# Performance work log

Hardware: AMD Instinct MI355X
Metric: run time of the kernel (lower is better)

## Reference

```python
import jax, jax.numpy as jnp
import numpy as np

K = 3      # kernel_size
PAD = 1    # padding
HID = 64   # hidden
EPS = 1e-5

def _unfold(x, H, W):
    # x: (B, CT, H, W) -> (B, CT, K*K, H*W); matches torch nn.Unfold channel-major layout
    xp = jnp.pad(x, ((0, 0), (0, 0), (PAD, PAD), (PAD, PAD)))
    patches = jnp.stack([xp[:, :, i:i + H, j:j + W]
                         for i in range(K) for j in range(K)], axis=2)
    B, CT = x.shape[:2]
    return patches.reshape(B, CT, K * K, H * W)

def _fold(y, H, W):
    # y: (B, CT, K*K, H*W) -> scatter-add overlapping patches -> (B, CT, H, W); matches F.fold
    B, CT = y.shape[:2]
    y = y.reshape(B, CT, K * K, H, W)
    out = jnp.zeros((B, CT, H + 2 * PAD, W + 2 * PAD), y.dtype)
    idx = 0
    for i in range(K):
        for j in range(K):
            out = out.at[:, :, i:i + H, j:j + W].add(y[:, :, idx])
            idx += 1
    return out[:, :, PAD:PAD + H, PAD:PAD + W]

def setup_inputs() -> dict:
    key = jax.random.key(0)
    ks = jax.random.split(key, 4)
    B, C, T, H, W = 8, 64, 4, 56, 56
    return {
        "x": jax.random.normal(ks[0], (B, C, T, H, W), jnp.float32),
        "w_in": jax.random.normal(ks[1], (3 * HID, C), jnp.float32) * (C ** -0.5),
        "b_in": jnp.zeros((3 * HID,), jnp.float32),
        "w_out": jax.random.normal(ks[2], (C, HID), jnp.float32) * (HID ** -0.5),
        "b_out": jnp.zeros((C,), jnp.float32),
        "gamma": jnp.ones((C,), jnp.float32),
        "beta": jnp.zeros((C,), jnp.float32),
    }

def reference(x, w_in, b_in, w_out, b_out, gamma, beta):
    B, C, T, H, W = x.shape
    k2 = K * K
    # 1x1x1 conv_in -> theta, phi, g
    h = jnp.einsum('oc,bcthw->bothw', w_in, x) + b_in[None, :, None, None, None]
    theta, phi, g = jnp.split(h, 3, axis=1)

    def unf(z):  # (B, HID, T, H, W) -> (B, HID, T*k2, H*W)
        z = z.reshape(B, HID * T, H, W)
        return _unfold(z, H, W).reshape(B, HID, T * k2, H * W)

    tu, pu, gu = unf(theta), unf(phi), unf(g)
    # per-spatial-location attention over T*k2 axis; dot_product normalization
    attn = jnp.einsum('bcts,bcps->btps', tu, pu) / (T * k2)
    out = jnp.einsum('btgs,bcgs->bcts', attn, gu)      # (B, HID, T*k2, H*W)
    out = out.reshape(B, HID * T, k2, H * W)
    out = _fold(out, H, W).reshape(B, HID, T, H, W)
    # 1x1x1 conv_out
    out = jnp.einsum('oc,bcthw->bothw', w_out, out) + b_out[None, :, None, None, None]
    # BatchNorm3d (training-mode batch statistics, biased variance)
    mu = out.mean(axis=(0, 2, 3, 4), keepdims=True)
    var = out.var(axis=(0, 2, 3, 4), keepdims=True)
    out = (out - mu) * jax.lax.rsqrt(var + EPS)
    out = out * gamma[None, :, None, None, None] + beta[None, :, None, None, None]
    return x + out
```

## Files before the change

kernel.cpp:

```cpp
#include <hip/hip_runtime.h>


typedef unsigned short u16;
typedef unsigned int u32;
using f32x4 = __attribute__((ext_vector_type(4))) float;
using bf16x8 = __attribute__((ext_vector_type(8))) short;

#define BB 8
#define TT 4
#define HH 56
#define HWD 3136
#define GROW 64
#define GPLANE 3584
#define NTOT 100352.0f

__device__ __forceinline__ float bf_lo(u32 u) { return __uint_as_float(u << 16); }
__device__ __forceinline__ float bf_hi(u32 u) { return __uint_as_float(u & 0xffff0000u); }
__device__ __forceinline__ float bf16u(u16 u) { return __uint_as_float(((u32)u) << 16); }
__device__ __forceinline__ u16 f2bf(float f) {
  u32 u = __float_as_uint(f);
  u32 r = (u + 0x7fffu + ((u >> 16) & 1u)) >> 16;
  return (u16)r;
}
__device__ __forceinline__ u32 pack2(float a, float b) {
  return (u32)f2bf(a) | ((u32)f2bf(b) << 16);
}
__device__ __forceinline__ int imax(int a, int b) { return a > b ? a : b; }
__device__ __forceinline__ int imin(int a, int b) { return a < b ? a : b; }
__device__ __forceinline__ float cntf(int d, int p) {
  int lo = imax(-1, imax(-1 - d, p - (HH - 1)));
  int hi = imin(1, imin(1 - d, p));
  int n = hi - lo + 1;
  return n > 0 ? (float)n : 0.f;
}

#define K1_XOFF 24576
__global__ __launch_bounds__(256, 4) void k_conv_in(const float* __restrict__ x,
                                                    const float* __restrict__ w_in,
                                                    const float* __restrict__ b_in,
                                                    u16* __restrict__ th, u16* __restrict__ ph,
                                                    u16* __restrict__ g2, float* __restrict__ stats) {
  __shared__ __align__(16) char sm[24576 + 8192];
  if (blockIdx.x == 0 && threadIdx.x < 128) stats[threadIdx.x] = 0.f;
  int bi0 = blockIdx.x;
  int bi = (bi0 & 7) * 196 + (bi0 >> 3);
  int bt = bi / 49, chunk = bi % 49;
  int b = bt >> 2, t = bt & 3;
  int p0 = chunk * 64;
  int tid = threadIdx.x;

#pragma unroll
  for (int it = 0; it < 12; ++it) {
    int task = it * 256 + tid;
    int o = task >> 4, c4 = (task & 15) * 4;
    float4 wv = *reinterpret_cast<const float4*>(&w_in[o * 64 + c4]);
    uint2 pv;
    pv.x = pack2(wv.x, wv.y);
    pv.y = pack2(wv.z, wv.w);
    *reinterpret_cast<uint2*>(sm + o * 128 + ((c4 * 2) ^ ((o & 7) << 4))) = pv;
  }
  const float* xb = x + ((size_t)b * 256 + t) * HWD + p0;
#pragma unroll
  for (int it = 0; it < 2; ++it) {
    int task = it * 256 + tid;
    int cp = task >> 4, p4 = task & 15;
    int c0 = cp * 2;
    float4 fa = *reinterpret_cast<const float4*>(&xb[(size_t)c0 * 4 * HWD + p4 * 4]);
    float4 fb = *reinterpret_cast<const float4*>(&xb[(size_t)(c0 + 1) * 4 * HWD + p4 * 4]);
    float va[4] = {fa.x, fa.y, fa.z, fa.w}, vb[4] = {fb.x, fb.y, fb.z, fb.w};
#pragma unroll
    for (int j = 0; j < 4; ++j) {
      int p = p4 * 4 + j;
      int slot = (p & 7) ^ ((p >> 2) & 7);
      *reinterpret_cast<u32*>(sm + K1_XOFF + p * 128 + ((c0 * 2) ^ (slot << 4))) = pack2(va[j], vb[j]);
    }
  }
  __syncthreads();

  int w = tid >> 6, lane = tid & 63, lr = lane & 15, lk = lane >> 4;
  f32x4 acc[3][4];
#pragma unroll
  for (int i = 0; i < 3; ++i)
#pragma unroll
    for (int n = 0; n < 4; ++n) acc[i][n] = (f32x4){0.f, 0.f, 0.f, 0.f};

#pragma unroll
  for (int kt = 0; kt < 2; ++kt) {
    bf16x8 af[3], bfr[4];
#pragma unroll
    for (int i = 0; i < 3; ++i) {
      int arow = (w * 3 + i) * 16 + lr;
      af[i] = *reinterpret_cast<const bf16x8*>(sm + arow * 128 + ((kt * 64 + lk * 16) ^ ((arow & 7) << 4)));
    }
#pragma unroll
    for (int n = 0; n < 4; ++n) {
      int brow = n * 16 + lr;
      int slot = (brow & 7) ^ ((brow >> 2) & 7);
      bfr[n] = *reinterpret_cast<const bf16x8*>(sm + K1_XOFF + brow * 128 + ((kt * 64 + lk * 16) ^ (slot << 4)));
    }
#pragma unroll
    for (int i = 0; i < 3; ++i)
#pragma unroll
      for (int n = 0; n < 4; ++n)
        acc[i][n] = __builtin_amdgcn_mfma_f32_16x16x32_bf16(af[i], bfr[n], acc[i][n], 0, 0, 0);
  }

#pragma unroll
  for (int i = 0; i < 3; ++i) {
    int mt = w * 3 + i;
    int ob = mt * 16 + lk * 4;
    int gsel = ob >> 6, o = ob & 63;
    float4 bv = *reinterpret_cast<const float4*>(&b_in[ob]);
    if (gsel < 2) {
      u16* og = gsel == 0 ? th : ph;
#pragma unroll
      for (int n = 0; n < 4; ++n) {
        int p = p0 + n * 16 + lr;
        f32x4 a = acc[i][n];
        uint2 v;
        v.x = pack2(a.x + bv.x, a.y + bv.y);
        v.y = pack2(a.z + bv.z, a.w + bv.w);
        *reinterpret_cast<uint2*>(&og[((size_t)bt * HWD + p) * 64 + o]) = v;
      }
    } else {
      float bb[4] = {bv.x, bv.y, bv.z, bv.w};
      int y0p = p0 / 56;
      int rel0 = p0 - y0p * 56;
#pragma unroll
      for (int n = 0; n < 4; ++n) {
        f32x4 a = acc[i][n];
        float aa[4] = {a.x, a.y, a.z, a.w};
        int rel = rel0 + n * 16 + lr;
        int cnd = rel >= 56;
        int off = (y0p + cnd) * GROW + (rel - (cnd ? 56 : 0)) + 2;
#pragma unroll
        for (int r = 0; r < 4; ++r)
          g2[(((size_t)b * 64 + o + r) * 4 + t) * GPLANE + off] = f2bf(aa[r] + bb[r]);
      }
    }
  }
}

#define PH_OFF 0
#define AS_OFF 0
#define G_OFF 32768
#define TH_OFF 65536
#define FOLD_OFF 65536
#define W_OFF 73728

__global__ __launch_bounds__(512, 4) void k_attn(const u16* __restrict__ th, const u16* __restrict__ ph,
                                                 const u16* __restrict__ g2,
                                                 const float* __restrict__ w_out,
                                                 const float* __restrict__ b_out,
                                                 u16* __restrict__ pre) {
  __shared__ __align__(16) char sm[81920];

  int bi0 = blockIdx.x;
  int bi = (bi0 & 7) * 196 + (bi0 >> 3);
  int b = bi / 196, tile = bi % 196;
  int ty = tile / 14, tx = tile % 14;
  int y0 = ty * 4, x0 = tx * 4;
  int tid = threadIdx.x;
  int w = tid >> 6, lane = tid & 63;
  int lr = lane & 15, lk = lane >> 4;

  for (int task = tid; task < 2048; task += 512) {
    int row = task >> 3, ch = task & 7;
    int rho = row >> 6, Z = row & 63, zy = Z >> 3, zx = Z & 7;
    int Y = y0 - 2 + zy, X = x0 - 2 + zx;
    uint4 v = make_uint4(0, 0, 0, 0);
    if ((unsigned)Y < HH && (unsigned)X < HH)
      v = *reinterpret_cast<const uint4*>(&ph[(((size_t)b * 4 + rho) * HWD + Y * HH + X) * 64 + ch * 8]);
    *reinterpret_cast<uint4*>(sm + PH_OFF + row * 128 + ((ch * 16) ^ ((row & 7) << 4))) = v;
  }
  {
    int row = tid >> 3, ch = tid & 7;
    int pos = row >> 2, tau = row & 3;
    int Y = y0 + (pos >> 2), X = x0 + (pos & 3);
    uint4 v = *reinterpret_cast<const uint4*>(&th[(((size_t)b * 4 + tau) * HWD + Y * HH + X) * 64 + ch * 8]);
    *reinterpret_cast<uint4*>(sm + TH_OFF + row * 128 + ((ch * 16) ^ ((row & 7) << 4))) = v;
  }
  for (int task = tid; task < 2048; task += 512) {
    int c = task >> 5, rho = (task >> 3) & 3, zy = task & 7;
    int Y = y0 - 2 + zy;
    uint2 lo = make_uint2(0, 0), hi = make_uint2(0, 0);
    if ((unsigned)Y < HH) {
      const u16* gb = g2 + (((size_t)b * 64 + c) * 4 + rho) * GPLANE + Y * GROW + x0;
      lo = *reinterpret_cast<const uint2*>(gb);
      hi = *reinterpret_cast<const uint2*>(gb + 4);
    }
    uint4 v = make_uint4(lo.x, lo.y, hi.x, hi.y);
    *reinterpret_cast<uint4*>(sm + G_OFF + c * 512 + ((16 * (rho * 8 + zy)) ^ ((c & 7) << 4))) = v;
  }
  {
    int o = tid >> 3, cg = tid & 7;
    float4 w0 = *reinterpret_cast<const float4*>(&w_out[o * 64 + cg * 8]);
    float4 w1 = *reinterpret_cast<const float4*>(&w_out[o * 64 + cg * 8 + 4]);
    uint4 wv = make_uint4(pack2(w0.x, w0.y), pack2(w0.z, w0.w), pack2(w1.x, w1.y), pack2(w1.z, w1.w));
    *reinterpret_cast<uint4*>(sm + W_OFF + o * 128 + ((cg * 16) ^ ((o & 7) << 4))) = wv;
  }
  __syncthreads();

  bf16x8 tb[4][2];
#pragma unroll
  for (int nt = 0; nt < 4; ++nt)
#pragma unroll
    for (int kt = 0; kt < 2; ++kt) {
      int row = nt * 16 + lr;
      tb[nt][kt] = *reinterpret_cast<const bf16x8*>(sm + TH_OFF + row * 128 + ((kt * 64 + lk * 16) ^ ((row & 7) << 4)));
    }
  f32x4 accA[2][4];
#pragma unroll
  for (int mi = 0; mi < 2; ++mi)
#pragma unroll
    for (int nt = 0; nt < 4; ++nt) accA[mi][nt] = (f32x4){0.f, 0.f, 0.f, 0.f};
  __builtin_amdgcn_s_setprio(1);
#pragma unroll
  for (int mi = 0; mi < 2; ++mi) {
    int mt = w * 2 + mi;
    int mrow = mt * 16 + lr;
    int p2 = (2 * mt) & 7;
#pragma unroll
    for (int kt = 0; kt < 2; ++kt) {
      bf16x8 af = *reinterpret_cast<const bf16x8*>(sm + PH_OFF + mrow * 128 + ((kt * 64 + lk * 16) ^ ((mrow & 7) << 4)));
#pragma unroll
      for (int nt = 0; nt < 4; ++nt) {
        if ((p2 == 0 && nt >= 2) || (p2 == 6 && nt < 2)) continue;
        accA[mi][nt] = __builtin_amdgcn_mfma_f32_16x16x32_bf16(af, tb[nt][kt], accA[mi][nt], 0, 0, 0);
      }
    }
  }
  __builtin_amdgcn_s_setprio(0);
  __syncthreads();

  {
    int px = lr >> 2;
#pragma unroll
    for (int mi = 0; mi < 2; ++mi) {
      int mbase = (w * 2 + mi) * 16 + lk * 4;
      int zy = (mbase >> 3) & 7;
      int zxb = mbase & 7;
      float cxv[4];
#pragma unroll
      for (int r = 0; r < 4; ++r) cxv[r] = cntf(zxb + r - 2 - px, x0 + px);
#pragma unroll
      for (int nt = 0; nt < 4; ++nt) {
        int n = nt * 16 + lr;
        float cyv = cntf(zy - 2 - nt, y0 + nt) * (1.f / 36.f);
        f32x4 a = accA[mi][nt];
        uint2 vv;
        vv.x = pack2(a.x * cyv * cxv[0], a.y * cyv * cxv[1]);
        vv.y = pack2(a.z * cyv * cxv[2], a.w * cyv * cxv[3]);
        *reinterpret_cast<uint2*>(sm + AS_OFF + n * 512 + ((mbase * 2) ^ ((n & 7) << 4))) = vv;
      }
    }
  }
  __syncthreads();

  int mtB = w & 3, ntb = (w >> 2) * 2;
  f32x4 accB[2];
  accB[0] = (f32x4){0.f, 0.f, 0.f, 0.f};
  accB[1] = (f32x4){0.f, 0.f, 0.f, 0.f};
  {
    int arow = mtB * 16 + lr;
    __builtin_amdgcn_s_setprio(1);
#pragma unroll
    for (int kt = 0; kt < 8; ++kt) {
      bf16x8 af = *reinterpret_cast<const bf16x8*>(sm + AS_OFF + arow * 512 + ((kt * 64 + lk * 16) ^ ((arow & 7) << 4)));
#pragma unroll
      for (int j = 0; j < 2; ++j) {
        int brow = (ntb + j) * 16 + lr;
        bf16x8 bfv = *reinterpret_cast<const bf16x8*>(sm + G_OFF + brow * 512 + ((kt * 64 + lk * 16) ^ ((brow & 7) << 4)));
        accB[j] = __builtin_amdgcn_mfma_f32_16x16x32_bf16(af, bfv, accB[j], 0, 0, 0);
      }
    }
    __builtin_amdgcn_s_setprio(0);
  }
#pragma unroll
  for (int j = 0; j < 2; ++j) {
    int n = (ntb + j) * 16 + lr;
#pragma unroll
    for (int r = 0; r < 4; ++r) {
      int m = mtB * 16 + lk * 4 + r;
      *reinterpret_cast<u16*>(sm + FOLD_OFF + m * 128 + ((n * 2) ^ ((m & 7) << 4))) = f2bf(accB[j][r]);
    }
  }
  __syncthreads();

  int mtC = w & 3, ntc = (w >> 2) * 2;
  f32x4 accC[2];
  accC[0] = (f32x4){0.f, 0.f, 0.f, 0.f};
  accC[1] = (f32x4){0.f, 0.f, 0.f, 0.f};
  {
    int arow = mtC * 16 + lr;
    __builtin_amdgcn_s_setprio(1);
#pragma unroll
    for (int kt = 0; kt < 2; ++kt) {
      bf16x8 af = *reinterpret_cast<const bf16x8*>(sm + W_OFF + arow * 128 + ((kt * 64 + lk * 16) ^ ((arow & 7) << 4)));
#pragma unroll
      for (int j = 0; j < 2; ++j) {
        int brow = (ntc + j) * 16 + lr;
        bf16x8 bfv = *reinterpret_cast<const bf16x8*>(sm + FOLD_OFF + brow * 128 + ((kt * 64 + lk * 16) ^ ((brow & 7) << 4)));
        accC[j] = __builtin_amdgcn_mfma_f32_16x16x32_bf16(af, bfv, accC[j], 0, 0, 0);
      }
    }
    __builtin_amdgcn_s_setprio(0);
  }
  {
    int o = mtC * 16 + lk * 4;
    float4 bo = *reinterpret_cast<const float4*>(&b_out[o]);
#pragma unroll
    for (int j = 0; j < 2; ++j) {
      int n = (ntc + j) * 16 + lr;
      int pos = n >> 2, tau = n & 3;
      int hw = (y0 + (pos >> 2)) * HH + x0 + (pos & 3);
      uint2 v;
      v.x = pack2(accC[j].x + bo.x, accC[j].y + bo.y);
      v.y = pack2(accC[j].z + bo.z, accC[j].w + bo.w);
      *reinterpret_cast<uint2*>(&pre[(((size_t)b * 4 + tau) * HWD + hw) * 64 + o]) = v;
    }
  }
}

__global__ __launch_bounds__(256) void k_stats(const u16* __restrict__ pre, float* __restrict__ stats) {
  __shared__ float rs[32][64], qs[32][64];
  int tid = threadIdx.x;
  int bi0 = blockIdx.x;
  int bi = (bi0 & 7) * 49 + (bi0 >> 3);
  int og = tid & 7, pg = tid >> 3;
  const uint4* p128 = reinterpret_cast<const uint4*>(pre);
  size_t base = (size_t)bi * 256 + pg * 8;
  float s[8] = {0, 0, 0, 0, 0, 0, 0, 0}, q[8] = {0, 0, 0, 0, 0, 0, 0, 0};
#pragma unroll
  for (int j = 0; j < 8; ++j) {
    uint4 v = p128[(base + j) * 8 + og];
    u32 uu[4] = {v.x, v.y, v.z, v.w};
#pragma unroll
    for (int k = 0; k < 4; ++k) {
      float a = bf_lo(uu[k]), c = bf_hi(uu[k]);
      s[k * 2] += a; q[k * 2] += a * a;
      s[k * 2 + 1] += c; q[k * 2 + 1] += c * c;
    }
  }
#pragma unroll
  for (int k = 0; k < 8; ++k) {
    rs[pg][og * 8 + k] = s[k];
    qs[pg][og * 8 + k] = q[k];
  }
  __syncthreads();
  if (tid < 64) {
    float ts = 0.f, tq = 0.f;
#pragma unroll
    for (int g = 0; g < 32; ++g) { ts += rs[g][tid]; tq += qs[g][tid]; }
    atomicAdd(&stats[tid], ts);
    atomicAdd(&stats[64 + tid], tq);
  }
}

__global__ __launch_bounds__(256) void k_final(const float* __restrict__ x, const u16* __restrict__ pre,
                                               const float* __restrict__ stats,
                                               const float* __restrict__ gamma,
                                               const float* __restrict__ beta,
                                               float* __restrict__ out) {
  __shared__ u32 pt[32][65];
  int bi0 = blockIdx.x;
  int bi = (bi0 & 7) * 196 + (bi0 >> 3);
  int bt = bi / 49, ck = bi % 49;
  int b = bt >> 2, t = bt & 3;
  int hw0 = ck * 64;
  int tid = threadIdx.x;
  int slot = tid & 15, c2 = tid >> 4;
  int p4 = slot * 4;

  float4 xv[2][2];
  size_t xb[2][2];
#pragma unroll
  for (int half = 0; half < 2; ++half) {
    int c0 = (c2 + half * 16) * 2;
    xb[half][0] = ((size_t)(b * 64 + c0) * 4 + t) * HWD + hw0 + p4;
    xb[half][1] = xb[half][0] + 4 * HWD;
    xv[half][0] = *reinterpret_cast<const float4*>(&x[xb[half][0]]);
    xv[half][1] = *reinterpret_cast<const float4*>(&x[xb[half][1]]);
  }

  const u32* src = reinterpret_cast<const u32*>(pre) + ((size_t)bt * HWD + hw0) * 32;
#pragma unroll
  for (int it = 0; it < 8; ++it) {
    int task = it * 256 + tid;
    int p = task >> 5, cu = task & 31;
    pt[cu][p] = src[p * 32 + cu];
  }
  __syncthreads();
  const float invN = 1.f / NTOT;
#pragma unroll
  for (int half = 0; half < 2; ++half) {
    int cp = c2 + half * 16;
    int c0 = cp * 2;
    float mu0 = stats[c0] * invN;
    float va0 = stats[64 + c0] * invN - mu0 * mu0;
    float s0 = rsqrtf(va0 + 1e-5f) * gamma[c0];
    float h0 = beta[c0] - mu0 * s0;
    float mu1 = stats[c0 + 1] * invN;
    float va1 = stats[64 + c0 + 1] * invN - mu1 * mu1;
    float s1 = rsqrtf(va1 + 1e-5f) * gamma[c0 + 1];
    float h1 = beta[c0 + 1] - mu1 * s1;
    uint4 pv = *reinterpret_cast<const uint4*>(&pt[cp][p4]);
    float4 x0v = xv[half][0], x1v = xv[half][1];
    float4 o0, o1;
    o0.x = x0v.x + bf_lo(pv.x) * s0 + h0;  o1.x = x1v.x + bf_hi(pv.x) * s1 + h1;
    o0.y = x0v.y + bf_lo(pv.y) * s0 + h0;  o1.y = x1v.y + bf_hi(pv.y) * s1 + h1;
    o0.z = x0v.z + bf_lo(pv.z) * s0 + h0;  o1.z = x1v.z + bf_hi(pv.z) * s1 + h1;
    o0.w = x0v.w + bf_lo(pv.w) * s0 + h0;  o1.w = x1v.w + bf_hi(pv.w) * s1 + h1;
    *reinterpret_cast<float4*>(&out[xb[half][0]]) = o0;
    *reinterpret_cast<float4*>(&out[xb[half][1]]) = o1;
  }
}

extern "C" void kernel_launch(void* const* d_in, const int* in_sizes, int n_in,
                              void* d_out, int out_size, void* d_ws, size_t ws_size,
                              hipStream_t stream) {
  const float* x = (const float*)d_in[0];
  const float* w_in = (const float*)d_in[1];
  const float* b_in = (const float*)d_in[2];
  const float* w_out = (const float*)d_in[3];
  const float* b_out = (const float*)d_in[4];
  const float* gamma = (const float*)d_in[5];
  const float* beta = (const float*)d_in[6];
  float* out = (float*)d_out;

  const size_t NE = (size_t)BB * TT * HWD * 64;
  const size_t NG = (size_t)BB * 64 * TT * GPLANE;
  u16* th = (u16*)d_ws;
  u16* ph = th + NE;
  u16* g2 = ph + NE;
  u16* pre = g2 + NG;
  float* stats = (float*)(pre + NE);

  k_conv_in<<<dim3(BB * TT * 49), dim3(256), 0, stream>>>(x, w_in, b_in, th, ph, g2, stats);
  k_attn<<<dim3(BB * 196), dim3(512), 0, stream>>>(th, ph, g2, w_out, b_out, pre);
  k_stats<<<dim3(392), dim3(256), 0, stream>>>(pre, stats);
  k_final<<<dim3(BB * TT * 49), dim3(256), 0, stream>>>(x, pre, stats, gamma, beta, out);
}
```

Baseline: 79.33 us.

## Make attention kernel persistent with register-prefetched next tile loads

The attention kernel now launches 512 persistent blocks, each looping over tiles with a stride of 64 instead of one block per tile. Global loads for the next tile are issued into registers right after the current tile's data lands in shared memory, so they overlap with the MFMA stages. Plain __syncthreads are replaced by an LDS-only wait plus s_barrier, so barriers do not drain the outstanding global prefetches. This adds register pressure (about 9 uint4 per thread) and leaves a tail imbalance, since 196 tiles split into 4 or 3 per slot.

Result: slower. 120.7 us (+52.2%).

```diff
diff --git a/kernel.cpp b/kernel.cpp
--- a/kernel.cpp
+++ b/kernel.cpp
@@ -32,6 +32,10 @@
   int hi = imin(1, imin(1 - d, p));
   int n = hi - lo + 1;
   return n > 0 ? (float)n : 0.f;
+}
+__device__ __forceinline__ void bar_lgkm() {
+  asm volatile("s_waitcnt lgkmcnt(0)" ::: "memory");
+  __builtin_amdgcn_s_barrier();
 }
 
 #define K1_XOFF 24576
@@ -155,43 +159,48 @@
                                                  u16* __restrict__ pre) {
   __shared__ __align__(16) char sm[81920];
 
-  int bi0 = blockIdx.x;
-  int bi = (bi0 & 7) * 196 + (bi0 >> 3);
-  int b = bi / 196, tile = bi % 196;
-  int ty = tile / 14, tx = tile % 14;
-  int y0 = ty * 4, x0 = tx * 4;
   int tid = threadIdx.x;
   int w = tid >> 6, lane = tid & 63;
   int lr = lane & 15, lk = lane >> 4;
-
-  for (int task = tid; task < 2048; task += 512) {
-    int row = task >> 3, ch = task & 7;
-    int rho = row >> 6, Z = row & 63, zy = Z >> 3, zx = Z & 7;
-    int Y = y0 - 2 + zy, X = x0 - 2 + zx;
-    uint4 v = make_uint4(0, 0, 0, 0);
-    if ((unsigned)Y < HH && (unsigned)X < HH)
-      v = *reinterpret_cast<const uint4*>(&ph[(((size_t)b * 4 + rho) * HWD + Y * HH + X) * 64 + ch * 8]);
-    *reinterpret_cast<uint4*>(sm + PH_OFF + row * 128 + ((ch * 16) ^ ((row & 7) << 4))) = v;
-  }
-  {
-    int row = tid >> 3, ch = tid & 7;
-    int pos = row >> 2, tau = row & 3;
-    int Y = y0 + (pos >> 2), X = x0 + (pos & 3);
-    uint4 v = *reinterpret_cast<const uint4*>(&th[(((size_t)b * 4 + tau) * HWD + Y * HH + X) * 64 + ch * 8]);
-    *reinterpret_cast<uint4*>(sm + TH_OFF + row * 128 + ((ch * 16) ^ ((row & 7) << 4))) = v;
-  }
-  for (int task = tid; task < 2048; task += 512) {
-    int c = task >> 5, rho = (task >> 3) & 3, zy = task & 7;
-    int Y = y0 - 2 + zy;
-    uint2 lo = make_uint2(0, 0), hi = make_uint2(0, 0);
-    if ((unsigned)Y < HH) {
-      const u16* gb = g2 + (((size_t)b * 64 + c) * 4 + rho) * GPLANE + Y * GROW + x0;
-      lo = *reinterpret_cast<const uint2*>(gb);
-      hi = *reinterpret_cast<const uint2*>(gb + 4);
-    }
-    uint4 v = make_uint4(lo.x, lo.y, hi.x, hi.y);
-    *reinterpret_cast<uint4*>(sm + G_OFF + c * 512 + ((16 * (rho * 8 + zy)) ^ ((c & 7) << 4))) = v;
-  }
+  int b = blockIdx.x & 7;
+  int slot = blockIdx.x >> 3;
+
+  uint4 pv[4], gv[4], thv;
+
+  auto issue_loads = [&](int y0, int x0) {
+#pragma unroll
+    for (int s = 0; s < 4; ++s) {
+      int task = s * 512 + tid;
+      int row = task >> 3, ch = task & 7;
+      int rho = row >> 6, Z = row & 63, zy = Z >> 3, zx = Z & 7;
+      int Y = y0 - 2 + zy, X = x0 - 2 + zx;
+      uint4 v = make_uint4(0, 0, 0, 0);
+      if ((unsigned)Y < HH && (unsigned)X < HH)
+        v = *reinterpret_cast<const uint4*>(&ph[(((size_t)b * 4 + rho) * HWD + Y * HH + X) * 64 + ch * 8]);
+      pv[s] = v;
+    }
+#pragma unroll
+    for (int s = 0; s < 4; ++s) {
+      int task = s * 512 + tid;
+      int c = task >> 5, rho = (task >> 3) & 3, zy = task & 7;
+      int Y = y0 - 2 + zy;
+      uint2 lo = make_uint2(0, 0), hi = make_uint2(0, 0);
+      if ((unsigned)Y < HH) {
+        const u16* gb = g2 + (((size_t)b * 64 + c) * 4 + rho) * GPLANE + Y * GROW + x0;
+        lo = *reinterpret_cast<const uint2*>(gb);
+        hi = *reinterpret_cast<const uint2*>(gb + 4);
+      }
+      gv[s] = make_uint4(lo.x, lo.y, hi.x, hi.y);
+    }
+    {
+      int row = tid >> 3, ch = tid & 7;
+      int pos = row >> 2, tau = row & 3;
+      int Y = y0 + (pos >> 2), X = x0 + (pos & 3);
+      thv = *reinterpret_cast<const uint4*>(&th[(((size_t)b * 4 + tau) * HWD + Y * HH + X) * 64 + ch * 8]);
+    }
+  };
+
+  issue_loads((slot / 14) * 4, (slot % 14) * 4);
   {
     int o = tid >> 3, cg = tid & 7;
     float4 w0 = *reinterpret_cast<const float4*>(&w_out[o * 64 + cg * 8]);
@@ -199,126 +208,151 @@
     uint4 wv = make_uint4(pack2(w0.x, w0.y), pack2(w0.z, w0.w), pack2(w1.x, w1.y), pack2(w1.z, w1.w));
     *reinterpret_cast<uint4*>(sm + W_OFF + o * 128 + ((cg * 16) ^ ((o & 7) << 4))) = wv;
   }
-  __syncthreads();
-
-  bf16x8 tb[4][2];
-#pragma unroll
-  for (int nt = 0; nt < 4; ++nt)
-#pragma unroll
-    for (int kt = 0; kt < 2; ++kt) {
-      int row = nt * 16 + lr;
-      tb[nt][kt] = *reinterpret_cast<const bf16x8*>(sm + TH_OFF + row * 128 + ((kt * 64 + lk * 16) ^ ((row & 7) << 4)));
-    }
-  f32x4 accA[2][4];
-#pragma unroll
-  for (int mi = 0; mi < 2; ++mi)
-#pragma unroll
-    for (int nt = 0; nt < 4; ++nt) accA[mi][nt] = (f32x4){0.f, 0.f, 0.f, 0.f};
-  __builtin_amdgcn_s_setprio(1);
-#pragma unroll
-  for (int mi = 0; mi < 2; ++mi) {
-    int mt = w * 2 + mi;
-    int mrow = mt * 16 + lr;
-    int p2 = (2 * mt) & 7;
-#pragma unroll
-    for (int kt = 0; kt < 2; ++kt) {
-      bf16x8 af = *reinterpret_cast<const bf16x8*>(sm + PH_OFF + mrow * 128 + ((kt * 64 + lk * 16) ^ ((mrow & 7) << 4)));
-#pragma unroll
-      for (int nt = 0; nt < 4; ++nt) {
-        if ((p2 == 0 && nt >= 2) || (p2 == 6 && nt < 2)) continue;
-        accA[mi][nt] = __builtin_amdgcn_mfma_f32_16x16x32_bf16(af, tb[nt][kt], accA[mi][nt], 0, 0, 0);
-      }
-    }
-  }
-  __builtin_amdgcn_s_setprio(0);
-  __syncthreads();
-
-  {
-    int px = lr >> 2;
+
+  for (int tile = slot; tile < 196; tile += 64) {
+    int y0 = (tile / 14) * 4, x0 = (tile % 14) * 4;
+
+#pragma unroll
+    for (int s = 0; s < 4; ++s) {
+      int task = s * 512 + tid;
+      int row = task >> 3, ch = task & 7;
+      *reinterpret_cast<uint4*>(sm + PH_OFF + row * 128 + ((ch * 16) ^ ((row & 7) << 4))) = pv[s];
+    }
+#pragma unroll
+    for (int s = 0; s < 4; ++s) {
+      int task = s * 512 + tid;
+      int c = task >> 5, rho = (task >> 3) & 3, zy = task & 7;
+      *reinterpret_cast<uint4*>(sm + G_OFF + c * 512 + ((16 * (rho * 8 + zy)) ^ ((c & 7) << 4))) = gv[s];
+    }
+    {
+      int row = tid >> 3, ch = tid & 7;
+      *reinterpret_cast<uint4*>(sm + TH_OFF + row * 128 + ((ch * 16) ^ ((row & 7) << 4))) = thv;
+    }
+    bar_lgkm();
+
+    int ntile = tile + 64;
+    if (ntile < 196) issue_loads((ntile / 14) * 4, (ntile % 14) * 4);
+
+    bf16x8 tb[4][2];
+#pragma unroll
+    for (int nt = 0; nt < 4; ++nt)
+#pragma unroll
+      for (int kt = 0; kt < 2; ++kt) {
+        int row = nt * 16 + lr;
+        tb[nt][kt] = *reinterpret_cast<const bf16x8*>(sm + TH_OFF + row * 128 + ((kt * 64 + lk * 16) ^ ((row & 7) << 4)));
+      }
+    f32x4 accA[2][4];
+#pragma unroll
+    for (int mi = 0; mi < 2; ++mi)
+#pragma unroll
+      for (int nt = 0; nt < 4; ++nt) accA[mi][nt] = (f32x4){0.f, 0.f, 0.f, 0.f};
+    __builtin_amdgcn_s_setprio(1);
 #pragma unroll
     for (int mi = 0; mi < 2; ++mi) {
-      int mbase = (w * 2 + mi) * 16 + lk * 4;
-      int zy = (mbase >> 3) & 7;
-      int zxb = mbase & 7;
-      float cxv[4];
-#pragma unroll
-      for (int r = 0; r < 4; ++r) cxv[r] = cntf(zxb + r - 2 - px, x0 + px);
-#pragma unroll
-      for (int nt = 0; nt < 4; ++nt) {
-        int n = nt * 16 + lr;
-        float cyv = cntf(zy - 2 - nt, y0 + nt) * (1.f / 36.f);
-        f32x4 a = accA[mi][nt];
-        uint2 vv;
-        vv.x = pack2(a.x * cyv * cxv[0], a.y * cyv * cxv[1]);
-        vv.y = pack2(a.z * cyv * cxv[2], a.w * cyv * cxv[3]);
-        *reinterpret_cast<uint2*>(sm + AS_OFF + n * 512 + ((mbase * 2) ^ ((n & 7) << 4))) = vv;
-      }
-    }
-  }
-  __syncthreads();
-
-  int mtB = w & 3, ntb = (w >> 2) * 2;
-  f32x4 accB[2];
-  accB[0] = (f32x4){0.f, 0.f, 0.f, 0.f};
-  accB[1] = (f32x4){0.f, 0.f, 0.f, 0.f};
-  {
-    int arow = mtB * 16 + lr;
-    __builtin_amdgcn_s_setprio(1);
-#pragma unroll
-    for (int kt = 0; kt < 8; ++kt) {
-      bf16x8 af = *reinterpret_cast<const bf16x8*>(sm + AS_OFF + arow * 512 + ((kt * 64 + lk * 16) ^ ((arow & 7) << 4)));
+      int mt = w * 2 + mi;
+      int mrow = mt * 16 + lr;
+      int p2 = (2 * mt) & 7;
+#pragma unroll
+      for (int kt = 0; kt < 2; ++kt) {
+        bf16x8 af = *reinterpret_cast<const bf16x8*>(sm + PH_OFF + mrow * 128 + ((kt * 64 + lk * 16) ^ ((mrow & 7) << 4)));
+#pragma unroll
+        for (int nt = 0; nt < 4; ++nt) {
+          if ((p2 == 0 && nt >= 2) || (p2 == 6 && nt < 2)) continue;
+          accA[mi][nt] = __builtin_amdgcn_mfma_f32_16x16x32_bf16(af, tb[nt][kt], accA[mi][nt], 0, 0, 0);
+        }
+      }
+    }
+    __builtin_amdgcn_s_setprio(0);
+    bar_lgkm();
+
+    {
+      int px = lr >> 2;
+#pragma unroll
+      for (int mi = 0; mi < 2; ++mi) {
+        int mbase = (w * 2 + mi) * 16 + lk * 4;
+        int zy = (mbase >> 3) & 7;
+        int zxb = mbase & 7;
+        float cxv[4];
+#pragma unroll
+        for (int r = 0; r < 4; ++r) cxv[r] = cntf(zxb + r - 2 - px, x0 + px);
+#pragma unroll
+        for (int nt = 0; nt < 4; ++nt) {
+          int n = nt * 16 + lr;
+          float cyv = cntf(zy - 2 - nt, y0 + nt) * (1.f / 36.f);
+          f32x4 a = accA[mi][nt];
+          uint2 vv;
+          vv.x = pack2(a.x * cyv * cxv[0], a.y * cyv * cxv[1]);
+          vv.y = pack2(a.z * cyv * cxv[2], a.w * cyv * cxv[3]);
+          *reinterpret_cast<uint2*>(sm + AS_OFF + n * 512 + ((mbase * 2) ^ ((n & 7) << 4))) = vv;
+        }
+      }
+    }
+    bar_lgkm();
+
+    int mtB = w & 3, ntb = (w >> 2) * 2;
+    f32x4 accB[2];
+    accB[0] = (f32x4){0.f, 0.f, 0.f, 0.f};
+    accB[1] = (f32x4){0.f, 0.f, 0.f, 0.f};
+    {
+      int arow = mtB * 16 + lr;
+      __builtin_amdgcn_s_setprio(1);
+#pragma unroll
+      for (int kt = 0; kt < 8; ++kt) {
+        bf16x8 af = *reinterpret_cast<const bf16x8*>(sm + AS_OFF + arow * 512 + ((kt * 64 + lk * 16) ^ ((arow & 7) << 4)));
+#pragma unroll
+        for (int j = 0; j < 2; ++j) {
+          int brow = (ntb + j) * 16 + lr;
+          bf16x8 bfv = *reinterpret_cast<const bf16x8*>(sm + G_OFF + brow * 512 + ((kt * 64 + lk * 16) ^ ((brow & 7) << 4)));
+          accB[j] = __builtin_amdgcn_mfma_f32_16x16x32_bf16(af, bfv, accB[j], 0, 0, 0);
+        }
+      }
+      __builtin_amdgcn_s_setprio(0);
+    }
+#pragma unroll
+    for (int j = 0; j < 2; ++j) {
+      int n = (ntb + j) * 16 + lr;
+#pragma unroll
+      for (int r = 0; r < 4; ++r) {
+        int m = mtB * 16 + lk * 4 + r;
+        *reinterpret_cast<u16*>(sm + FOLD_OFF + m * 128 + ((n * 2) ^ ((m & 7) << 4))) = f2bf(accB[j][r]);
+      }
+    }
+    bar_lgkm();
+
+    int mtC = w & 3, ntc = (w >> 2) * 2;
+    f32x4 accC[2];
+    accC[0] = (f32x4){0.f, 0.f, 0.f, 0.f};
+    accC[1] = (f32x4){0.f, 0.f, 0.f, 0.f};
+    {
+      int arow = mtC * 16 + lr;
+      __builtin_amdgcn_s_setprio(1);
+#pragma unroll
+      for (int kt = 0; kt < 2; ++kt) {
+        bf16x8 af = *reinterpret_cast<const bf16x8*>(sm + W_OFF + arow * 128 + ((kt * 64 + lk * 16) ^ ((arow & 7) << 4)));
+#pragma unroll
+        for (int j = 0; j < 2; ++j) {
+          int brow = (ntc + j) * 16 + lr;
+          bf16x8 bfv = *reinterpret_cast<const bf16x8*>(sm + FOLD_OFF + brow * 128 + ((kt * 64 + lk * 16) ^ ((brow & 7) << 4)));
+          accC[j] = __builtin_amdgcn_mfma_f32_16x16x32_bf16(af, bfv, accC[j], 0, 0, 0);
+        }
+      }
+      __builtin_amdgcn_s_setprio(0);
+    }
+    {
+      int o = mtC * 16 + lk * 4;
+      float4 bo = *reinterpret_cast<const float4*>(&b_out[o]);
 #pragma unroll
       for (int j = 0; j < 2; ++j) {
-        int brow = (ntb + j) * 16 + lr;
-        bf16x8 bfv = *reinterpret_cast<const bf16x8*>(sm + G_OFF + brow * 512 + ((kt * 64 + lk * 16) ^ ((brow & 7) << 4)));
-        accB[j] = __builtin_amdgcn_mfma_f32_16x16x32_bf16(af, bfv, accB[j], 0, 0, 0);
-      }
-    }
-    __builtin_amdgcn_s_setprio(0);
-  }
-#pragma unroll
-  for (int j = 0; j < 2; ++j) {
-    int n = (ntb + j) * 16 + lr;
-#pragma unroll
-    for (int r = 0; r < 4; ++r) {
-      int m = mtB * 16 + lk * 4 + r;
-      *reinterpret_cast<u16*>(sm + FOLD_OFF + m * 128 + ((n * 2) ^ ((m & 7) << 4))) = f2bf(accB[j][r]);
-    }
-  }
-  __syncthreads();
-
-  int mtC = w & 3, ntc = (w >> 2) * 2;
-  f32x4 accC[2];
-  accC[0] = (f32x4){0.f, 0.f, 0.f, 0.f};
-  accC[1] = (f32x4){0.f, 0.f, 0.f, 0.f};
-  {
-    int arow = mtC * 16 + lr;
-    __builtin_amdgcn_s_setprio(1);
-#pragma unroll
-    for (int kt = 0; kt < 2; ++kt) {
-      bf16x8 af = *reinterpret_cast<const bf16x8*>(sm + W_OFF + arow * 128 + ((kt * 64 + lk * 16) ^ ((arow & 7) << 4)));
-#pragma unroll
-      for (int j = 0; j < 2; ++j) {
-        int brow = (ntc + j) * 16 + lr;
-        bf16x8 bfv = *reinterpret_cast<const bf16x8*>(sm + FOLD_OFF + brow * 128 + ((kt * 64 + lk * 16) ^ ((brow & 7) << 4)));
-        accC[j] = __builtin_amdgcn_mfma_f32_16x16x32_bf16(af, bfv, accC[j], 0, 0, 0);
-      }
-    }
-    __builtin_amdgcn_s_setprio(0);
-  }
-  {
-    int o = mtC * 16 + lk * 4;
-    float4 bo = *reinterpret_cast<const float4*>(&b_out[o]);
-#pragma unroll
-    for (int j = 0; j < 2; ++j) {
-      int n = (ntc + j) * 16 + lr;
-      int pos = n >> 2, tau = n & 3;
-      int hw = (y0 + (pos >> 2)) * HH + x0 + (pos & 3);
-      uint2 v;
-      v.x = pack2(accC[j].x + bo.x, accC[j].y + bo.y);
-      v.y = pack2(accC[j].z + bo.z, accC[j].w + bo.w);
-      *reinterpret_cast<uint2*>(&pre[(((size_t)b * 4 + tau) * HWD + hw) * 64 + o]) = v;
-    }
+        int n = (ntc + j) * 16 + lr;
+        int pos = n >> 2, tau = n & 3;
+        int hw = (y0 + (pos >> 2)) * HH + x0 + (pos & 3);
+        uint2 v;
+        v.x = pack2(accC[j].x + bo.x, accC[j].y + bo.y);
+        v.y = pack2(accC[j].z + bo.z, accC[j].w + bo.w);
+        *reinterpret_cast<uint2*>(&pre[(((size_t)b * 4 + tau) * HWD + hw) * 64 + o]) = v;
+      }
+    }
+    bar_lgkm();
   }
 }
 
@@ -437,7 +471,7 @@
   float* stats = (float*)(pre + NE);
 
   k_conv_in<<<dim3(BB * TT * 49), dim3(256), 0, stream>>>(x, w_in, b_in, th, ph, g2, stats);
-  k_attn<<<dim3(BB * 196), dim3(512), 0, stream>>>(th, ph, g2, w_out, b_out, pre);
+  k_attn<<<dim3(512), dim3(512), 0, stream>>>(th, ph, g2, w_out, b_out, pre);
   k_stats<<<dim3(392), dim3(256), 0, stream>>>(pre, stats);
   k_final<<<dim3(BB * TT * 49), dim3(256), 0, stream>>>(x, pre, stats, gamma, beta, out);
 }
```
